# Performance work log

Measured on AMD Instinct MI355X. Metric: run time of the kernel, lower is better.

Reference implementation:

```python
import jax, jax.numpy as jnp
import numpy as np

L = 0.24          # lambda step size
K = 0.03          # exp(log 0.03), conductance scale used by forward
NITER = 500       # ctor Niter
DEPS = 0.1


def _g(x, k):
    # Perona-Malik conductance: 1 / (1 + |x^2| / k^2); x real so |x*x| == x*x
    return 1.0 / (1.0 + (x * x) / (k * k))


def setup_inputs() -> dict:
    key = jax.random.key(0)
    k1, k2 = jax.random.split(key)
    guide = jax.random.normal(k1, (2, 3, 512, 512), dtype=jnp.float32)
    initial = jax.random.uniform(k2, (2, 1, 512, 512), dtype=jnp.float32)
    return {"guide": guide, "initial": initial}


def reference(guide, initial):
    # shift branch (jit-safe): forward adds deps if initial.min() <= deps, subtracts at end
    shift = jnp.where(jnp.min(initial) <= DEPS, DEPS, 0.0).astype(initial.dtype)
    depth0 = initial + shift

    # conductance coefficients from guide (mean abs channel gradient), shapes:
    # cv: [B,1,H-1,W], ch: [B,1,H,W-1]
    cv = _g(jnp.mean(jnp.abs(guide[:, :, 1:, :] - guide[:, :, :-1, :]), axis=1, keepdims=True), K)
    ch = _g(jnp.mean(jnp.abs(guide[:, :, :, 1:] - guide[:, :, :, :-1]), axis=1, keepdims=True), K)

    def step(I, _):
        # both diffs computed from the same I (matches torch: dv, dh read before writes;
        # the in-place +/- updates commute, so functional adds give identical math)
        dv = I[:, :, 1:, :] - I[:, :, :-1, :]
        dh = I[:, :, :, 1:] - I[:, :, :, :-1]
        tv = L * cv * dv
        th = L * ch * dh
        I = I.at[:, :, 1:, :].add(-tv)
        I = I.at[:, :, :-1, :].add(tv)
        I = I.at[:, :, :, 1:].add(-th)
        I = I.at[:, :, :, :-1].add(th)
        return I, None

    depth, _ = jax.lax.scan(step, depth0, None, length=NITER)
    y_pred = depth - shift
    return (y_pred, cv, ch)
```

## Files before the change

### kernel.cpp

```cpp
#include <hip/hip_runtime.h>


#define HH 512
#define WW 512
#define NB 2
static constexpr float LAM   = 0.24f;
static constexpr float KCOND = 0.03f;
static constexpr float DEPS_ = 0.1f;
static constexpr int IMG      = HH * WW;
static constexpr int N_DEPTH  = NB * IMG;
static constexpr int CV_PER_B = (HH - 1) * WW;
static constexpr int CH_PER_B = HH * (WW - 1);
static constexpr int N_CV     = NB * CV_PER_B;
static constexpr int N_CH     = NB * CH_PER_B;

static constexpr int T_FUSE = 10, NSS = 50;
static constexpr int TILE_W = 64, TILE_H = 32;
static constexpr int HALO_X = 12, HALO_Y = 10;
static constexpr int RW = TILE_W + 2 * HALO_X;
static constexpr int RH = TILE_H + 2 * HALO_Y;
static constexpr int NQ_ROW = RW / 4;
static constexpr int NQUAD  = NQ_ROW * RH;
static constexpr int SSZ    = (RH + 2) * RW;

static constexpr int NU_ROW = RW / 4;
static constexpr int NU_COL = RH / 2;
static constexpr int NUNIT  = NU_ROW * NU_COL;
static constexpr int NTF    = 576;

static constexpr int S_LDS    = 92;
static constexpr int ROWS_SZ  = (RH + 2) * S_LDS;
static constexpr int TRASH_OFF = ROWS_SZ;
static constexpr int EDGE_OFF = ROWS_SZ + S_LDS;
static constexpr int EDGE_ENT = 580;
static constexpr int BUF_SZ   = EDGE_OFF + EDGE_ENT * 4;

static constexpr int QPT_F = 5;

__device__ __forceinline__ unsigned fkey(float f) {
    unsigned u = __float_as_uint(f);
    return (u & 0x80000000u) ? ~u : (u | 0x80000000u);
}
__device__ __forceinline__ float kinv(unsigned k) {
    return __uint_as_float((k & 0x80000000u) ? (k & 0x7fffffffu) : ~k);
}

__device__ __forceinline__ float2 cohload8(const float* p) {
    unsigned long long u = __hip_atomic_load(
        reinterpret_cast<const unsigned long long*>(p),
        __ATOMIC_RELAXED, __HIP_MEMORY_SCOPE_AGENT);
    union { unsigned long long u; float2 f; } c; c.u = u;
    return c.f;
}
__device__ __forceinline__ void cohstore8(float* p, float a, float b) {
    union { unsigned long long u; float f[2]; } c;
    c.f[0] = a; c.f[1] = b;
    __hip_atomic_store(reinterpret_cast<unsigned long long*>(p), c.u,
                       __ATOMIC_RELAXED, __HIP_MEMORY_SCOPE_AGENT);
}

__global__ void init_key_kernel(unsigned* key, unsigned* flags) {
    if (threadIdx.x == 0) *key = 0xFFFFFFFFu;
    flags[threadIdx.x] = 0u;
}

static constexpr int NCO_BLK = (N_CV + N_CH + 255) / 256;
__global__ void coeff_min_kernel(const float* __restrict__ g,
                                 const float* __restrict__ ini,
                                 float* __restrict__ cv, float* __restrict__ chh,
                                 unsigned* __restrict__ key) {
    constexpr float kk = KCOND * KCOND;
    if ((int)blockIdx.x >= NCO_BLK) {
        int bid = blockIdx.x - NCO_BLK;
        float m = 3.4e38f;
        for (int idx = bid * 256 + threadIdx.x; idx < N_DEPTH; idx += 256 * 256)
            m = fminf(m, ini[idx]);
        for (int off = 32; off > 0; off >>= 1) m = fminf(m, __shfl_down(m, off, 64));
        __shared__ float sm[4];
        int lane = threadIdx.x & 63, wv = threadIdx.x >> 6;
        if (lane == 0) sm[wv] = m;
        __syncthreads();
        if (threadIdx.x == 0) {
            float mm = fminf(fminf(sm[0], sm[1]), fminf(sm[2], sm[3]));
            atomicMin(key, fkey(mm));
        }
        return;
    }
    int idx = blockIdx.x * 256 + threadIdx.x;
    if (idx < N_CV) {
        int b = idx / CV_PER_B;
        int r = idx - b * CV_PER_B;
        int i = r >> 9, j = r & (WW - 1);
        const float* gb = g + b * 3 * IMG + i * WW + j;
        float s = 0.f;
#pragma unroll
        for (int c = 0; c < 3; ++c) s += fabsf(gb[c * IMG + WW] - gb[c * IMG]);
        float m = s / 3.0f;
        cv[idx] = 1.0f / (1.0f + (m * m) / kk);
    } else if (idx < N_CV + N_CH) {
        int t = idx - N_CV;
        int b = t / CH_PER_B;
        int r = t - b * CH_PER_B;
        int i = r / (WW - 1);
        int j = r - i * (WW - 1);
        const float* gb = g + b * 3 * IMG + i * WW + j;
        float s = 0.f;
#pragma unroll
        for (int c = 0; c < 3; ++c) s += fabsf(gb[c * IMG + 1] - gb[c * IMG]);
        float m = s / 3.0f;
        chh[t] = 1.0f / (1.0f + (m * m) / kk);
    }
}

__global__ __launch_bounds__(NTF, 1) void diffuse_persist(
    const float* __restrict__ initial, float* __restrict__ out_y,
    float* __restrict__ bufA, float* __restrict__ bufB,
    const float* __restrict__ cv_g, const float* __restrict__ ch_g,
    const unsigned* __restrict__ key, unsigned* __restrict__ flags) {
    __shared__ float sb[2][BUF_SZ];
    const int blk = blockIdx.x;
    const int b   = blk >> 7, t = blk & 127;
    const int ty  = t >> 3, tx = t & 7;
    const int y0  = ty * TILE_H;
    const int x0  = tx * TILE_W;
    const float shift = (kinv(*key) <= DEPS_) ? DEPS_ : 0.f;
    const int tid = threadIdx.x;

    const bool act = tid < NUNIT;
    const int  uc  = act ? tid : 0;
    const int  pr  = uc / NU_ROW;
    const int  px  = uc - pr * NU_ROW;
    const int  x   = px * 4;
    const int  r0  = 2 * pr, r1 = r0 + 1;
    int roff0 = (r0 + 1) * S_LDS + x;
    int roff1 = roff0 + S_LDS;
    if (!act) { roff0 = TRASH_OFF + (tid & 3) * 8; roff1 = roff0 + 4; }
    const int e_w  = EDGE_OFF + (tid + 1) * 4;
    const int e_lf = EDGE_OFF + tid * 4 + 2;
    const int e_rt = EDGE_OFF + (tid + 2) * 4;

    const int gy0 = y0 - HALO_Y + r0, gy1 = gy0 + 1;
    const int gx  = x0 - HALO_X + x;
    const bool gx_in = (gx >= 0) && (gx <= WW - 4);
    const bool in0 = act && gx_in && (gy0 >= 0) && (gy0 < HH);
    const bool in1 = act && gx_in && (gy1 >= 0) && (gy1 < HH);
    const int goff0 = in0 ? (gy0 * WW + gx) : 0;
    const int goff1 = in1 ? (gy1 * WW + gx) : 0;
    const bool is_int = act && (r0 >= HALO_Y) && (r1 < HALO_Y + TILE_H) &&
                        (x >= HALO_X) && (x < HALO_X + TILE_W);

    const float* cvb = cv_g + b * CV_PER_B;
    const float* chb = ch_g + b * CH_PER_B;
    float ca[4], cm[4], cb[4], h0[5], h1[5];
#pragma unroll
    for (int j = 0; j < 4; ++j) {
        int gxx = gx + j;
        bool gxo = (gxx >= 0) && (gxx < WW);
        bool a_ok = act && (r0 >= 1) && (gy0 >= 1) && (gy0 <= HH - 1) && gxo;
        ca[j] = a_ok ? LAM * cvb[(gy0 - 1) * WW + gxx] : 0.f;
        bool m_ok = act && (gy1 >= 1) && (gy1 <= HH - 1) && gxo;
        cm[j] = m_ok ? LAM * cvb[(gy1 - 1) * WW + gxx] : 0.f;
        bool b_ok = act && (r1 <= RH - 2) && (gy1 + 1 >= 1) && (gy1 + 1 <= HH - 1) && gxo;
        cb[j] = b_ok ? LAM * cvb[gy1 * WW + gxx] : 0.f;
    }
#pragma unroll
    for (int jj = 0; jj < 5; ++jj) {
        int xe = x + jj, gxe = gx + jj;
        bool e_ok = (xe >= 1) && (xe <= RW - 1) && (gxe >= 1) && (gxe < WW);
        bool ok0 = act && e_ok && (gy0 >= 0) && (gy0 < HH);
        h0[jj] = ok0 ? LAM * chb[gy0 * (WW - 1) + (gxe - 1)] : 0.f;
        bool ok1 = act && e_ok && (gy1 >= 0) && (gy1 < HH);
        h1[jj] = ok1 ? LAM * chb[gy1 * (WW - 1) + (gxe - 1)] : 0.f;
    }

    int nbr = -1;
    if (tid < 8) {
        int d  = tid + (tid >= 4 ? 1 : 0);
        int dy = d / 3 - 1, dx = d % 3 - 1;
        int ny = ty + dy, nx = tx + dx;
        if (ny >= 0 && ny < 16 && nx >= 0 && nx < 8)
            nbr = (b << 7) + (ny << 3) + nx;
    }

    float v0[4] = {0.f, 0.f, 0.f, 0.f}, v1[4] = {0.f, 0.f, 0.f, 0.f};
    const float* ib = initial + b * IMG;
    if (in0) {
        float4 tv = *reinterpret_cast<const float4*>(ib + goff0);
        v0[0] = tv.x + shift; v0[1] = tv.y + shift; v0[2] = tv.z + shift; v0[3] = tv.w + shift;
    }
    if (in1) {
        float4 tv = *reinterpret_cast<const float4*>(ib + goff1);
        v1[0] = tv.x + shift; v1[1] = tv.y + shift; v1[2] = tv.z + shift; v1[3] = tv.w + shift;
    }

    for (int i = tid; i < S_LDS; i += NTF) {
        sb[0][i] = 0.f; sb[0][(RH + 1) * S_LDS + i] = 0.f;
        sb[1][i] = 0.f; sb[1][(RH + 1) * S_LDS + i] = 0.f;
    }
    if (tid == 0) {
        float4 z{0.f, 0.f, 0.f, 0.f};
        *reinterpret_cast<float4*>(&sb[0][EDGE_OFF]) = z;
        *reinterpret_cast<float4*>(&sb[1][EDGE_OFF]) = z;
        *reinterpret_cast<float4*>(&sb[0][EDGE_OFF + 577 * 4]) = z;
        *reinterpret_cast<float4*>(&sb[1][EDGE_OFF + 577 * 4]) = z;
    }
    *reinterpret_cast<float4*>(&sb[0][roff0]) = float4{v0[0], v0[1], v0[2], v0[3]};
    *reinterpret_cast<float4*>(&sb[0][roff1]) = float4{v1[0], v1[1], v1[2], v1[3]};
    *reinterpret_cast<float4*>(&sb[0][e_w])   = float4{v0[0], v1[0], v0[3], v1[3]};
    __syncthreads();

    for (int k = 0; k < NSS; ++k) {
        if (k > 0) {
            if (nbr >= 0) {
                while (__hip_atomic_load(&flags[nbr], __ATOMIC_RELAXED,
                                         __HIP_MEMORY_SCOPE_AGENT) < (unsigned)k) {}
            }
            __syncthreads();
            asm volatile("" ::: "memory");
            const float* srcb = ((k & 1) ? bufA : bufB) + b * IMG;
            if (act && !is_int) {
                float2 a0{0.f, 0.f}, b0{0.f, 0.f}, a1{0.f, 0.f}, b1{0.f, 0.f};
                if (in0) { a0 = cohload8(srcb + goff0); b0 = cohload8(srcb + goff0 + 2); }
                if (in1) { a1 = cohload8(srcb + goff1); b1 = cohload8(srcb + goff1 + 2); }
                v0[0] = a0.x; v0[1] = a0.y; v0[2] = b0.x; v0[3] = b0.y;
                v1[0] = a1.x; v1[1] = a1.y; v1[2] = b1.x; v1[3] = b1.y;
                *reinterpret_cast<float4*>(&sb[0][roff0]) =
                    float4{v0[0], v0[1], v0[2], v0[3]};
                *reinterpret_cast<float4*>(&sb[0][roff1]) =
                    float4{v1[0], v1[1], v1[2], v1[3]};
                *reinterpret_cast<float4*>(&sb[0][e_w]) =
                    float4{v0[0], v1[0], v0[3], v1[3]};
            }
            __syncthreads();
        }

        int cur = 0;
        for (int it = 0; it < T_FUSE; ++it) {
            const float* s = sb[cur];
            float2 lfp = *reinterpret_cast<const float2*>(&s[e_lf]);
            float2 rtp = *reinterpret_cast<const float2*>(&s[e_rt]);
            float4 up = *reinterpret_cast<const float4*>(&s[roff0 - S_LDS]);
            float4 dn = *reinterpret_cast<const float4*>(&s[roff1 + S_LDS]);

            float n0[4], n1[4];
            n0[0] = v0[0] - ca[0] * (v0[0] - up.x) + cm[0] * (v1[0] - v0[0])
                          - h0[0] * (v0[0] - lfp.x) + h0[1] * (v0[1] - v0[0]);
            n0[1] = v0[1] - ca[1] * (v0[1] - up.y) + cm[1] * (v1[1] - v0[1])
                          - h0[1] * (v0[1] - v0[0]) + h0[2] * (v0[2] - v0[1]);
            n0[2] = v0[2] - ca[2] * (v0[2] - up.z) + cm[2] * (v1[2] - v0[2])
                          - h0[2] * (v0[2] - v0[1]) + h0[3] * (v0[3] - v0[2]);
            n0[3] = v0[3] - ca[3] * (v0[3] - up.w) + cm[3] * (v1[3] - v0[3])
                          - h0[3] * (v0[3] - v0[2]) + h0[4] * (rtp.x - v0[3]);
            n1[0] = v1[0] - cm[0] * (v1[0] - v0[0]) + cb[0] * (dn.x - v1[0])
                          - h1[0] * (v1[0] - lfp.y) + h1[1] * (v1[1] - v1[0]);
            n1[1] = v1[1] - cm[1] * (v1[1] - v0[1]) + cb[1] * (dn.y - v1[1])
                          - h1[1] * (v1[1] - v1[0]) + h1[2] * (v1[2] - v1[1]);
            n1[2] = v1[2] - cm[2] * (v1[2] - v0[2]) + cb[2] * (dn.z - v1[2])
                          - h1[2] * (v1[2] - v1[1]) + h1[3] * (v1[3] - v1[2]);
            n1[3] = v1[3] - cm[3] * (v1[3] - v0[3]) + cb[3] * (dn.w - v1[3])
                          - h1[3] * (v1[3] - v1[2]) + h1[4] * (rtp.y - v1[3]);

            int nxt = cur ^ 1;
            float* d = sb[nxt];
            *reinterpret_cast<float4*>(&d[roff0]) = float4{n0[0], n0[1], n0[2], n0[3]};
            *reinterpret_cast<float4*>(&d[roff1]) = float4{n1[0], n1[1], n1[2], n1[3]};
            *reinterpret_cast<float4*>(&d[e_w])   = float4{n0[0], n1[0], n0[3], n1[3]};
            v0[0] = n0[0]; v0[1] = n0[1]; v0[2] = n0[2]; v0[3] = n0[3];
            v1[0] = n1[0]; v1[1] = n1[1]; v1[2] = n1[2]; v1[3] = n1[3];
            cur = nxt;
            __syncthreads();
        }

        if (k == NSS - 1) {
            float* dstb = out_y + b * IMG;
            if (is_int) {
                float4 o0{v0[0] - shift, v0[1] - shift, v0[2] - shift, v0[3] - shift};
                float4 o1{v1[0] - shift, v1[1] - shift, v1[2] - shift, v1[3] - shift};
                *reinterpret_cast<float4*>(dstb + goff0) = o0;
                *reinterpret_cast<float4*>(dstb + goff1) = o1;
            }
        } else {
            float* dstb = ((k & 1) ? bufB : bufA) + b * IMG;
            if (is_int) {
                cohstore8(dstb + goff0,     v0[0], v0[1]);
                cohstore8(dstb + goff0 + 2, v0[2], v0[3]);
                cohstore8(dstb + goff1,     v1[0], v1[1]);
                cohstore8(dstb + goff1 + 2, v1[2], v1[3]);
            }
            asm volatile("s_waitcnt vmcnt(0)" ::: "memory");
            __syncthreads();
            if (tid == 0)
                __hip_atomic_store(&flags[blk], (unsigned)(k + 1),
                                   __ATOMIC_RELAXED, __HIP_MEMORY_SCOPE_AGENT);
        }
    }
}

template <bool ADD_SHIFT, bool SUB_SHIFT>
__global__ __launch_bounds__(256, 1) void step_fused(
    const float* __restrict__ src, float* __restrict__ dst,
    const float* __restrict__ cv_g, const float* __restrict__ ch_g,
    const unsigned* __restrict__ key) {
    __shared__ float sb[2][SSZ];
    const int blk = blockIdx.x;
    const int b = blk >> 7, t = blk & 127;
    const int y0 = (t >> 3) * TILE_H, x0 = (t & 7) * TILE_W;
    const float* cvb = cv_g + b * CV_PER_B;
    const float* chb = ch_g + b * CH_PER_B;
    const float* srcb = src + b * IMG;
    float* dstb = dst + b * IMG;
    float shift = 0.f;
    if (ADD_SHIFT || SUB_SHIFT) shift = (kinv(*key) <= DEPS_) ? DEPS_ : 0.f;
    const int tid = threadIdx.x;
    float v[QPT_F][4], cu[QPT_F][4], cd[QPT_F][4], chq[QPT_F][5];
    int roff[QPT_F], rr[QPT_F], xx[QPT_F];
    bool act[QPT_F];
#pragma unroll
    for (int q = 0; q < QPT_F; ++q) {
        int qi = tid + q * 256;
        act[q] = qi < NQUAD;
        int qc = act[q] ? qi : 0;
        int r = qc / NQ_ROW;
        int x = (qc - r * NQ_ROW) * 4;
        rr[q] = r; xx[q] = x;
        roff[q] = (r + 1) * RW + x;
        int gy = y0 - HALO_Y + r, gx = x0 - HALO_X + x;
        bool gy_in = (gy >= 0) && (gy < HH);
#pragma unroll
        for (int j = 0; j < 4; ++j) {
            int gxx = gx + j;
            bool gx_in = (gxx >= 0) && (gxx < WW);
            bool vin = act[q] && gy_in && gx_in;
            float val = vin ? srcb[gy * WW + gxx] : 0.f;
            if (ADD_SHIFT) val += shift;
            v[q][j] = vin ? val : 0.f;
            bool up_ok = act[q] && (r >= 1) && (gy >= 1) && (gy < HH) && gx_in;
            cu[q][j] = up_ok ? LAM * cvb[(gy - 1) * WW + gxx] : 0.f;
            bool dn_ok = act[q] && (r <= RH - 2) && (gy >= 0) && (gy < HH - 1) && gx_in;
            cd[q][j] = dn_ok ? LAM * cvb[gy * WW + gxx] : 0.f;
        }
#pragma unroll
        for (int jj = 0; jj < 5; ++jj) {
            int xe = x + jj, gxe = gx + jj;
            bool ok = act[q] && (xe >= 1) && (xe <= RW - 1) && gy_in &&
                      (gxe >= 1) && (gxe < WW);
            chq[q][jj] = ok ? LAM * chb[gy * (WW - 1) + (gxe - 1)] : 0.f;
        }
    }
    for (int i = tid; i < RW; i += 256) {
        sb[0][i] = 0.f; sb[0][(RH + 1) * RW + i] = 0.f;
        sb[1][i] = 0.f; sb[1][(RH + 1) * RW + i] = 0.f;
    }
#pragma unroll
    for (int q = 0; q < QPT_F; ++q)
        if (act[q])
            *reinterpret_cast<float4*>(&sb[0][roff[q]]) =
                float4{v[q][0], v[q][1], v[q][2], v[q][3]};
    __syncthreads();
    int cur = 0;
    for (int it = 0; it < T_FUSE; ++it) {
        float nv[QPT_F][4];
#pragma unroll
        for (int q = 0; q < QPT_F; ++q) {
            const float* s = sb[cur];
            float4 up = *reinterpret_cast<const float4*>(&s[roff[q] - RW]);
            float4 dn = *reinterpret_cast<const float4*>(&s[roff[q] + RW]);
            float lf = s[roff[q] - 1];
            float rt = s[roff[q] + 4];
            float c0 = v[q][0], c1 = v[q][1], c2 = v[q][2], c3 = v[q][3];
            nv[q][0] = c0 - cu[q][0] * (c0 - up.x) + cd[q][0] * (dn.x - c0)
                          - chq[q][0] * (c0 - lf) + chq[q][1] * (c1 - c0);
            nv[q][1] = c1 - cu[q][1] * (c1 - up.y) + cd[q][1] * (dn.y - c1)
                          - chq[q][1] * (c1 - c0) + chq[q][2] * (c2 - c1);
            nv[q][2] = c2 - cu[q][2] * (c2 - up.z) + cd[q][2] * (dn.z - c2)
                          - chq[q][2] * (c2 - c1) + chq[q][3] * (c3 - c2);
            nv[q][3] = c3 - cu[q][3] * (c3 - up.w) + cd[q][3] * (dn.w - c3)
                          - chq[q][3] * (c3 - c2) + chq[q][4] * (rt - c3);
        }
        int nxt = cur ^ 1;
#pragma unroll
        for (int q = 0; q < QPT_F; ++q) {
            if (act[q])
                *reinterpret_cast<float4*>(&sb[nxt][roff[q]]) =
                    float4{nv[q][0], nv[q][1], nv[q][2], nv[q][3]};
            v[q][0] = nv[q][0]; v[q][1] = nv[q][1];
            v[q][2] = nv[q][2]; v[q][3] = nv[q][3];
        }
        cur = nxt;
        __syncthreads();
    }
#pragma unroll
    for (int q = 0; q < QPT_F; ++q) {
        if (!act[q]) continue;
        int r = rr[q], x = xx[q];
        if (r >= HALO_Y && r < HALO_Y + TILE_H && x >= HALO_X && x < HALO_X + TILE_W) {
            int gy = y0 - HALO_Y + r, gx = x0 - HALO_X + x;
            float4 o{v[q][0], v[q][1], v[q][2], v[q][3]};
            if (SUB_SHIFT) { o.x -= shift; o.y -= shift; o.z -= shift; o.w -= shift; }
            *reinterpret_cast<float4*>(dstb + gy * WW + gx) = o;
        }
    }
}

extern "C" void kernel_launch(void* const* d_in, const int* in_sizes, int n_in,
                              void* d_out, int out_size, void* d_ws, size_t ws_size,
                              hipStream_t stream) {
    const float* guide   = (const float*)d_in[0];
    const float* initial = (const float*)d_in[1];
    float* out    = (float*)d_out;
    float* out_y  = out;
    float* out_cv = out + N_DEPTH;
    float* out_ch = out + N_DEPTH + N_CV;

    unsigned* key = (unsigned*)d_ws;
    float* wsf    = (float*)d_ws;
    float* bufA   = wsf + 64;
    float* bufB   = bufA + N_DEPTH;
    unsigned* flags = (unsigned*)(bufB + N_DEPTH);

    const size_t need = (size_t)(64 + 2 * N_DEPTH + 256) * 4;
    const bool fast = ws_size >= need;

    hipLaunchKernelGGL(init_key_kernel, dim3(1), dim3(256), 0, stream, key,
                       fast ? flags : (unsigned*)d_ws + 1);
    hipLaunchKernelGGL(coeff_min_kernel, dim3(NCO_BLK + 256), dim3(256), 0, stream,
                       guide, initial, out_cv, out_ch, key);

    if (fast) {
        const float* a0 = initial;
        float* a1 = out_y;
        float* a2 = bufA;
        float* a3 = bufB;
        const float* a4 = out_cv;
        const float* a5 = out_ch;
        const unsigned* a6 = key;
        unsigned* a7 = flags;
        void* kargs[] = {&a0, &a1, &a2, &a3, &a4, &a5, &a6, &a7};
        hipError_t ce = hipLaunchCooperativeKernel(
            (const void*)diffuse_persist, dim3(256), dim3(NTF), kargs, 0, stream);
        if (ce == hipSuccess) return;
    }

    float* bufs[2] = {bufA, bufB};
    for (int k = 0; k < NSS; ++k) {
        const float* src = (k == 0) ? initial : bufs[(k + 1) & 1];
        float*       dst = (k == NSS - 1) ? out_y : bufs[k & 1];
        if (k == 0)
            hipLaunchKernelGGL((step_fused<true, false>), dim3(256), dim3(256), 0,
                               stream, src, dst, out_cv, out_ch, key);
        else if (k == NSS - 1)
            hipLaunchKernelGGL((step_fused<false, true>), dim3(256), dim3(256), 0,
                               stream, src, dst, out_cv, out_ch, key);
        else
            hipLaunchKernelGGL((step_fused<false, false>), dim3(256), dim3(256), 0,
                               stream, src, dst, out_cv, out_ch, key);
    }
}
```

Baseline: 470.3 us.

## Drop init kernel via per-block min partials; store only seam cells each sync

Removes the separate init kernel by having the min-reduction blocks write per-block partial minima and clear the sync flags. The persistent kernel then reduces those partials itself at startup to derive the shift. Each temporal-block iteration now stores only the seam region of a tile's interior to global memory instead of the whole interior, since neighbours only read halo cells near tile edges. This cuts launch overhead and global store traffic. It relies on the inner region never being read by neighbouring tiles, and on the final output being written by a different path.

```diff
diff --git a/kernel.cpp b/kernel.cpp
--- a/kernel.cpp
+++ b/kernel.cpp
@@ -34,16 +34,9 @@
 static constexpr int EDGE_OFF = ROWS_SZ + S_LDS;
 static constexpr int EDGE_ENT = 580;
 static constexpr int BUF_SZ   = EDGE_OFF + EDGE_ENT * 4;
+static constexpr int MIN_SCR  = TRASH_OFF + 40;
 
 static constexpr int QPT_F = 5;
-
-__device__ __forceinline__ unsigned fkey(float f) {
-    unsigned u = __float_as_uint(f);
-    return (u & 0x80000000u) ? ~u : (u | 0x80000000u);
-}
-__device__ __forceinline__ float kinv(unsigned k) {
-    return __uint_as_float((k & 0x80000000u) ? (k & 0x7fffffffu) : ~k);
-}
 
 __device__ __forceinline__ float2 cohload8(const float* p) {
     unsigned long long u = __hip_atomic_load(
@@ -59,19 +52,16 @@
                        __ATOMIC_RELAXED, __HIP_MEMORY_SCOPE_AGENT);
 }
 
-__global__ void init_key_kernel(unsigned* key, unsigned* flags) {
-    if (threadIdx.x == 0) *key = 0xFFFFFFFFu;
-    flags[threadIdx.x] = 0u;
-}
-
 static constexpr int NCO_BLK = (N_CV + N_CH + 255) / 256;
 __global__ void coeff_min_kernel(const float* __restrict__ g,
                                  const float* __restrict__ ini,
                                  float* __restrict__ cv, float* __restrict__ chh,
-                                 unsigned* __restrict__ key) {
+                                 float* __restrict__ partials,
+                                 unsigned* __restrict__ flags) {
     constexpr float kk = KCOND * KCOND;
     if ((int)blockIdx.x >= NCO_BLK) {
         int bid = blockIdx.x - NCO_BLK;
+        if (threadIdx.x == 0) flags[bid] = 0u;
         float m = 3.4e38f;
         for (int idx = bid * 256 + threadIdx.x; idx < N_DEPTH; idx += 256 * 256)
             m = fminf(m, ini[idx]);
@@ -80,10 +70,8 @@
         int lane = threadIdx.x & 63, wv = threadIdx.x >> 6;
         if (lane == 0) sm[wv] = m;
         __syncthreads();
-        if (threadIdx.x == 0) {
-            float mm = fminf(fminf(sm[0], sm[1]), fminf(sm[2], sm[3]));
-            atomicMin(key, fkey(mm));
-        }
+        if (threadIdx.x == 0)
+            partials[bid] = fminf(fminf(sm[0], sm[1]), fminf(sm[2], sm[3]));
         return;
     }
     int idx = blockIdx.x * 256 + threadIdx.x;
@@ -112,18 +100,29 @@
     }
 }
 
+__global__ void key_from_partials(const float* __restrict__ partials,
+                                  float* __restrict__ keyf) {
+    float m = partials[threadIdx.x];
+    for (int off = 32; off > 0; off >>= 1) m = fminf(m, __shfl_down(m, off, 64));
+    __shared__ float sm[4];
+    int lane = threadIdx.x & 63, wv = threadIdx.x >> 6;
+    if (lane == 0) sm[wv] = m;
+    __syncthreads();
+    if (threadIdx.x == 0)
+        keyf[0] = fminf(fminf(sm[0], sm[1]), fminf(sm[2], sm[3]));
+}
+
 __global__ __launch_bounds__(NTF, 1) void diffuse_persist(
     const float* __restrict__ initial, float* __restrict__ out_y,
     float* __restrict__ bufA, float* __restrict__ bufB,
     const float* __restrict__ cv_g, const float* __restrict__ ch_g,
-    const unsigned* __restrict__ key, unsigned* __restrict__ flags) {
+    const float* __restrict__ partials, unsigned* __restrict__ flags) {
     __shared__ float sb[2][BUF_SZ];
     const int blk = blockIdx.x;
     const int b   = blk >> 7, t = blk & 127;
     const int ty  = t >> 3, tx = t & 7;
     const int y0  = ty * TILE_H;
     const int x0  = tx * TILE_W;
-    const float shift = (kinv(*key) <= DEPS_) ? DEPS_ : 0.f;
     const int tid = threadIdx.x;
 
     const bool act = tid < NUNIT;
@@ -148,6 +147,10 @@
     const int goff1 = in1 ? (gy1 * WW + gx) : 0;
     const bool is_int = act && (r0 >= HALO_Y) && (r1 < HALO_Y + TILE_H) &&
                         (x >= HALO_X) && (x < HALO_X + TILE_W);
+    const int rel_r = r0 - HALO_Y, rel_x = x - HALO_X;
+    const bool is_inner = is_int && (rel_r >= 10) && (rel_r <= 20) &&
+                          (rel_x >= 12) && (rel_x <= 48);
+    const bool store_seam = is_int && !is_inner;
 
     const float* cvb = cv_g + b * CV_PER_B;
     const float* chb = ch_g + b * CH_PER_B;
@@ -186,11 +189,19 @@
     const float* ib = initial + b * IMG;
     if (in0) {
         float4 tv = *reinterpret_cast<const float4*>(ib + goff0);
-        v0[0] = tv.x + shift; v0[1] = tv.y + shift; v0[2] = tv.z + shift; v0[3] = tv.w + shift;
+        v0[0] = tv.x; v0[1] = tv.y; v0[2] = tv.z; v0[3] = tv.w;
     }
     if (in1) {
         float4 tv = *reinterpret_cast<const float4*>(ib + goff1);
-        v1[0] = tv.x + shift; v1[1] = tv.y + shift; v1[2] = tv.z + shift; v1[3] = tv.w + shift;
+        v1[0] = tv.x; v1[1] = tv.y; v1[2] = tv.z; v1[3] = tv.w;
+    }
+
+    {
+        float pm = 3.4e38f;
+        if (tid < 256) pm = partials[tid];
+        for (int off = 32; off > 0; off >>= 1)
+            pm = fminf(pm, __shfl_down(pm, off, 64));
+        if (tid < 256 && (tid & 63) == 0) sb[0][MIN_SCR + (tid >> 6)] = pm;
     }
 
     for (int i = tid; i < S_LDS; i += NTF) {
@@ -204,6 +215,14 @@
         *reinterpret_cast<float4*>(&sb[0][EDGE_OFF + 577 * 4]) = z;
         *reinterpret_cast<float4*>(&sb[1][EDGE_OFF + 577 * 4]) = z;
     }
+    __syncthreads();
+
+    const float mm = fminf(fminf(sb[0][MIN_SCR], sb[0][MIN_SCR + 1]),
+                           fminf(sb[0][MIN_SCR + 2], sb[0][MIN_SCR + 3]));
+    const float shift = (mm <= DEPS_) ? DEPS_ : 0.f;
+    if (in0) { v0[0] += shift; v0[1] += shift; v0[2] += shift; v0[3] += shift; }
+    if (in1) { v1[0] += shift; v1[1] += shift; v1[2] += shift; v1[3] += shift; }
+
     *reinterpret_cast<float4*>(&sb[0][roff0]) = float4{v0[0], v0[1], v0[2], v0[3]};
     *reinterpret_cast<float4*>(&sb[0][roff1]) = float4{v1[0], v1[1], v1[2], v1[3]};
     *reinterpret_cast<float4*>(&sb[0][e_w])   = float4{v0[0], v1[0], v0[3], v1[3]};
@@ -281,7 +300,7 @@
             }
         } else {
             float* dstb = ((k & 1) ? bufB : bufA) + b * IMG;
-            if (is_int) {
+            if (store_seam) {
                 cohstore8(dstb + goff0,     v0[0], v0[1]);
                 cohstore8(dstb + goff0 + 2, v0[2], v0[3]);
                 cohstore8(dstb + goff1,     v1[0], v1[1]);
@@ -300,7 +319,7 @@
 __global__ __launch_bounds__(256, 1) void step_fused(
     const float* __restrict__ src, float* __restrict__ dst,
     const float* __restrict__ cv_g, const float* __restrict__ ch_g,
-    const unsigned* __restrict__ key) {
+    const float* __restrict__ keyf) {
     __shared__ float sb[2][SSZ];
     const int blk = blockIdx.x;
     const int b = blk >> 7, t = blk & 127;
@@ -310,7 +329,7 @@
     const float* srcb = src + b * IMG;
     float* dstb = dst + b * IMG;
     float shift = 0.f;
-    if (ADD_SHIFT || SUB_SHIFT) shift = (kinv(*key) <= DEPS_) ? DEPS_ : 0.f;
+    if (ADD_SHIFT || SUB_SHIFT) shift = (keyf[0] <= DEPS_) ? DEPS_ : 0.f;
     const int tid = threadIdx.x;
     float v[QPT_F][4], cu[QPT_F][4], cd[QPT_F][4], chq[QPT_F][5];
     int roff[QPT_F], rr[QPT_F], xx[QPT_F];
@@ -412,19 +431,18 @@
     float* out_cv = out + N_DEPTH;
     float* out_ch = out + N_DEPTH + N_CV;
 
-    unsigned* key = (unsigned*)d_ws;
     float* wsf    = (float*)d_ws;
+    float* keyf   = wsf;
     float* bufA   = wsf + 64;
     float* bufB   = bufA + N_DEPTH;
     unsigned* flags = (unsigned*)(bufB + N_DEPTH);
-
-    const size_t need = (size_t)(64 + 2 * N_DEPTH + 256) * 4;
+    float* partials = (float*)(flags + 256);
+
+    const size_t need = (size_t)(64 + 2 * N_DEPTH + 512) * 4;
     const bool fast = ws_size >= need;
 
-    hipLaunchKernelGGL(init_key_kernel, dim3(1), dim3(256), 0, stream, key,
-                       fast ? flags : (unsigned*)d_ws + 1);
     hipLaunchKernelGGL(coeff_min_kernel, dim3(NCO_BLK + 256), dim3(256), 0, stream,
-                       guide, initial, out_cv, out_ch, key);
+                       guide, initial, out_cv, out_ch, partials, flags);
 
     if (fast) {
         const float* a0 = initial;
@@ -433,7 +451,7 @@
         float* a3 = bufB;
         const float* a4 = out_cv;
         const float* a5 = out_ch;
-        const unsigned* a6 = key;
+        const float* a6 = partials;
         unsigned* a7 = flags;
         void* kargs[] = {&a0, &a1, &a2, &a3, &a4, &a5, &a6, &a7};
         hipError_t ce = hipLaunchCooperativeKernel(
@@ -441,18 +459,20 @@
         if (ce == hipSuccess) return;
     }
 
+    hipLaunchKernelGGL(key_from_partials, dim3(1), dim3(256), 0, stream,
+                       partials, keyf);
     float* bufs[2] = {bufA, bufB};
     for (int k = 0; k < NSS; ++k) {
         const float* src = (k == 0) ? initial : bufs[(k + 1) & 1];
         float*       dst = (k == NSS - 1) ? out_y : bufs[k & 1];
         if (k == 0)
             hipLaunchKernelGGL((step_fused<true, false>), dim3(256), dim3(256), 0,
-                               stream, src, dst, out_cv, out_ch, key);
+                               stream, src, dst, out_cv, out_ch, keyf);
         else if (k == NSS - 1)
             hipLaunchKernelGGL((step_fused<false, true>), dim3(256), dim3(256), 0,
-                               stream, src, dst, out_cv, out_ch, key);
+                               stream, src, dst, out_cv, out_ch, keyf);
         else
             hipLaunchKernelGGL((step_fused<false, false>), dim3(256), dim3(256), 0,
-                               stream, src, dst, out_cv, out_ch, key);
-    }
-}
+                               stream, src, dst, out_cv, out_ch, keyf);
+    }
+}
```

Result: no change. 461.3 us (-1.9%).
